# Kernel optimization log

Measured on AMD Instinct MI355X. Metric: run time of the kernel, lower is better.

The kernel has to match this reference:

```python
import jax, jax.numpy as jnp
import numpy as np

BN_EPS = 1e-5

def _haar_details(x):
    # pywt.dwt2(x, 'haar') details for even H, W.
    # Block [[p, q], [r, s]] with p = x[2i,2j], q = x[2i,2j+1], r = x[2i+1,2j], s = x[2i+1,2j+1].
    # cH ('da'): detail along rows, approx along cols; cV ('ad'); cD ('dd').
    B, C, H, W = x.shape
    xb = x.reshape(B, C, H // 2, 2, W // 2, 2)
    p = xb[:, :, :, 0, :, 0]
    q = xb[:, :, :, 0, :, 1]
    r = xb[:, :, :, 1, :, 0]
    s = xb[:, :, :, 1, :, 1]
    cH = (p + q - r - s) * 0.5
    cV = (p - q + r - s) * 0.5
    cD = (p - q - r + s) * 0.5
    return cH, cV, cD

def setup_inputs() -> dict:
    key = jax.random.key(0)
    k1, k2 = jax.random.split(key)
    B, C, H, W = 8, 256, 128, 128
    x = jax.random.normal(k1, (B, C, H, W), dtype=jnp.float32)
    conv_w = jax.random.normal(k2, (C, 4 * C), dtype=jnp.float32) * (1.0 / np.sqrt(4 * C))
    gamma = jnp.ones((C,), dtype=jnp.float32)
    beta = jnp.zeros((C,), dtype=jnp.float32)
    return {"x": x, "conv_w": conv_w, "gamma": gamma, "beta": beta}

def reference(x, conv_w, gamma, beta):
    B, C, H, W = x.shape
    # Original detaches the wavelet branch (CPU numpy path) -> stop_gradient.
    xs = jax.lax.stop_gradient(x)
    cH, cV, cD = _haar_details(xs)
    # Bilinear upsample to (H, W); jax.image.resize bilinear == torch align_corners=False.
    up = lambda t: jax.image.resize(t, (B, C, H, W), method="bilinear")
    enhanced = jnp.concatenate([x, up(cH), up(cV), up(cD)], axis=1)  # [B, 4C, H, W]
    # 1x1 conv, no bias.
    y = jnp.einsum("bchw,oc->bohw", enhanced, conv_w)  # [B, C, H, W]
    # BatchNorm2d, training-mode (batch statistics, biased variance).
    mean = jnp.mean(y, axis=(0, 2, 3), keepdims=True)
    var = jnp.mean((y - mean) ** 2, axis=(0, 2, 3), keepdims=True)
    y_hat = (y - mean) * jax.lax.rsqrt(var + BN_EPS)
    out = jax.nn.relu(y_hat * gamma[None, :, None, None] + beta[None, :, None, None])
    return out
```

## Files before the change

### kernel.cpp

```cpp
#include <hip/hip_runtime.h>
#include <hip/hip_bf16.h>

typedef __bf16 bf16;
typedef __bf16 bf16x8 __attribute__((ext_vector_type(8)));
typedef float  f32x4  __attribute__((ext_vector_type(4)));

#define AS1 __attribute__((address_space(1)))
#define AS3 __attribute__((address_space(3)))

__device__ __forceinline__ void load16_to_lds(const bf16* g, bf16* l) {
    __builtin_amdgcn_global_load_lds((const AS1 unsigned int*)g,
                                     (AS3 unsigned int*)l, 16, 0, 0);
}

__global__ __launch_bounds__(256) void prep_w(const float* __restrict__ w,
                                              bf16* __restrict__ wb) {
    int i = blockIdx.x * 256 + threadIdx.x;
    wb[i] = (bf16)w[i];
}

__global__ __launch_bounds__(256) void pass0(const float* __restrict__ x,
                                             bf16* __restrict__ xt,
                                             bf16* __restrict__ cT) {
    __shared__ bf16 tile[64 * 264];
    const int bid = blockIdx.x;
    const int wt = bid & 3, j = (bid >> 2) & 63, b = bid >> 8;
    const int t = threadIdx.x;
    const int w0 = wt * 32;

    for (int i = 0; i < 16; ++i) {
        int g = i * 256 + t;
        int c = g >> 4;
        int rem = g & 15;
        int dlt = rem >> 3, w4 = rem & 7;
        const float4 v = *(const float4*)(x +
            ((((size_t)b * 256 + c) * 128 + (2 * j + dlt)) * 128 + w0 + w4 * 4));
        int pos = dlt * 32 + w4 * 4;
        tile[(pos + 0) * 264 + c] = (bf16)v.x;
        tile[(pos + 1) * 264 + c] = (bf16)v.y;
        tile[(pos + 2) * 264 + c] = (bf16)v.z;
        tile[(pos + 3) * 264 + c] = (bf16)v.w;
    }
    __syncthreads();

    for (int i = 0; i < 8; ++i) {
        int q = i * 256 + t;
        int cq = q & 31, pos = q >> 5;
        int dlt = pos >> 5, w = pos & 31;
        bf16x8 v = *(const bf16x8*)&tile[pos * 264 + cq * 8];
        int h = 2 * j + dlt, wg = w0 + w;
        *(bf16x8*)(xt + (((size_t)b * 16384 + h * 128 + wg) * 256 + cq * 8)) = v;
    }

    for (int i = 0; i < 2; ++i) {
        int q = i * 256 + t;
        int cq = q & 31, kc = q >> 5;
        bf16x8 vp = *(const bf16x8*)&tile[(2 * kc) * 264 + cq * 8];
        bf16x8 vq = *(const bf16x8*)&tile[(2 * kc + 1) * 264 + cq * 8];
        bf16x8 vr = *(const bf16x8*)&tile[(32 + 2 * kc) * 264 + cq * 8];
        bf16x8 vs = *(const bf16x8*)&tile[(33 + 2 * kc) * 264 + cq * 8];
        bf16x8 oh, ov, od;
        #pragma unroll
        for (int e = 0; e < 8; ++e) {
            float p = (float)vp[e], qq = (float)vq[e];
            float r = (float)vr[e], s = (float)vs[e];
            oh[e] = (bf16)(0.5f * (p + qq - r - s));
            ov[e] = (bf16)(0.5f * (p - qq + r - s));
            od[e] = (bf16)(0.5f * (p - qq - r + s));
        }
        size_t row = ((size_t)b * 4096 + j * 64 + wt * 16 + kc) * 768;
        *(bf16x8*)(cT + row + 0 * 256 + cq * 8) = oh;
        *(bf16x8*)(cT + row + 1 * 256 + cq * 8) = ov;
        *(bf16x8*)(cT + row + 2 * 256 + cq * 8) = od;
    }
}

__global__ __launch_bounds__(256) void gemm_bt(const bf16* __restrict__ W,
                                               const bf16* __restrict__ X,
                                               bf16* __restrict__ Y,
                                               int K, int kofs, int mshift) {
    __shared__ bf16 Wt[128 * 32];
    __shared__ bf16 Xt[128 * 32];
    const int t = threadIdx.x;
    const int wave = t >> 6, lane = t & 63;
    const int quad = lane >> 4, l16 = lane & 15;
    const int m0 = blockIdx.x * 128, o0 = blockIdx.y * 128;
    const int wo = (wave >> 1) * 64, wm = (wave & 1) * 64;
    const int Mplane = 1 << mshift;
    const int r_in = lane >> 2;
    const int cch = lane & 3;

    f32x4 acc[4][4] = {};

    const bf16* wbase = W + (size_t)o0 * 1024 + kofs;
    const bf16* xbase = X + (size_t)m0 * K;

    for (int kk = 0; kk < K; kk += 32) {
        #pragma unroll
        for (int i = 0; i < 2; ++i) {
            int rblk = wave * 2 + i;
            int row = rblk * 16 + r_in;
            load16_to_lds(wbase + (size_t)row * 1024 + kk + cch * 8,
                          &Wt[rblk * 512 + lane * 8]);
            load16_to_lds(xbase + (size_t)row * K + kk + cch * 8,
                          &Xt[rblk * 512 + lane * 8]);
        }
        __syncthreads();
        bf16x8 af[4], bfr[4];
        #pragma unroll
        for (int i = 0; i < 4; ++i)
            af[i] = *(const bf16x8*)&Wt[(wo + i * 16 + l16) * 32 + quad * 8];
        #pragma unroll
        for (int jj = 0; jj < 4; ++jj)
            bfr[jj] = *(const bf16x8*)&Xt[(wm + jj * 16 + l16) * 32 + quad * 8];
        #pragma unroll
        for (int i = 0; i < 4; ++i)
            #pragma unroll
            for (int jj = 0; jj < 4; ++jj)
                acc[i][jj] = __builtin_amdgcn_mfma_f32_16x16x32_bf16(
                    af[i], bfr[jj], acc[i][jj], 0, 0, 0);
        __syncthreads();
    }

    #pragma unroll
    for (int i = 0; i < 4; ++i) {
        int o = o0 + wo + i * 16 + quad * 4;
        #pragma unroll
        for (int jj = 0; jj < 4; ++jj) {
            int m = m0 + wm + jj * 16 + l16;
            int bb = m >> mshift;
            int mp = m & (Mplane - 1);
            bf16* yp = Y + ((size_t)bb * 256 + o) * Mplane + mp;
            #pragma unroll
            for (int r = 0; r < 4; ++r)
                yp[(size_t)r * Mplane] = (bf16)acc[i][jj][r];
        }
    }
}

__device__ __forceinline__ float up_val(const float* zs, int p) {
    int h = p >> 7, w = p & 127;
    int j0 = h >> 1, k0 = w >> 1;
    int jn = (h & 1) ? min(j0 + 1, 63) : max(j0 - 1, 0);
    int kn = (w & 1) ? min(k0 + 1, 63) : max(k0 - 1, 0);
    float zmm = zs[j0 * 64 + k0], zmn = zs[j0 * 64 + kn];
    float znm = zs[jn * 64 + k0], znn = zs[jn * 64 + kn];
    return 0.5625f * zmm + 0.1875f * (zmn + znm) + 0.0625f * znn;
}

__device__ __forceinline__ void load_zplane(const bf16* zp, float* zs, int t) {
    for (int i = 0; i < 2; ++i) {
        int idx = (i * 256 + t) * 8;
        bf16x8 v = *(const bf16x8*)(zp + idx);
        #pragma unroll
        for (int e = 0; e < 8; ++e) zs[idx + e] = (float)v[e];
    }
}

__global__ __launch_bounds__(256) void stats_k(const bf16* __restrict__ y1,
                                               const bf16* __restrict__ z,
                                               float* __restrict__ stats) {
    __shared__ float zs[4096];
    __shared__ float red[8];
    const int bid = blockIdx.x;
    const int o = bid & 255, b = bid >> 8;
    const int t = threadIdx.x;
    const bf16* zp = z + ((size_t)b * 256 + o) * 4096;
    const bf16* yp = y1 + ((size_t)b * 256 + o) * 16384;
    load_zplane(zp, zs, t);
    __syncthreads();
    float s = 0.f, ss = 0.f;
    for (int i = 0; i < 64; ++i) {
        int p = i * 256 + t;
        float y = (float)yp[p] + up_val(zs, p);
        s += y; ss += y * y;
    }
    #pragma unroll
    for (int off = 32; off > 0; off >>= 1) {
        s += __shfl_down(s, off);
        ss += __shfl_down(ss, off);
    }
    if ((t & 63) == 0) { red[t >> 6] = s; red[4 + (t >> 6)] = ss; }
    __syncthreads();
    if (t == 0) {
        atomicAdd(&stats[o],       red[0] + red[1] + red[2] + red[3]);
        atomicAdd(&stats[256 + o], red[4] + red[5] + red[6] + red[7]);
    }
}

__global__ __launch_bounds__(256) void finalize_k(float* __restrict__ stats,
                                                  const float* __restrict__ gamma,
                                                  const float* __restrict__ beta) {
    int o = threadIdx.x;
    const float n = 131072.f;
    float mean = stats[o] / n;
    float var = stats[256 + o] / n - mean * mean;
    float rstd = rsqrtf(var + 1e-5f);
    float sc = rstd * gamma[o];
    stats[512 + o] = sc;
    stats[768 + o] = beta[o] - mean * sc;
}

__global__ __launch_bounds__(256) void apply_k(const bf16* __restrict__ y1,
                                               const bf16* __restrict__ z,
                                               const float* __restrict__ stats,
                                               float* __restrict__ out) {
    __shared__ float zs[4096];
    const int bid = blockIdx.x;
    const int o = bid & 255, b = bid >> 8;
    const int t = threadIdx.x;
    const bf16* zp = z + ((size_t)b * 256 + o) * 4096;
    const bf16* yp = y1 + ((size_t)b * 256 + o) * 16384;
    float* op = out + ((size_t)b * 256 + o) * 16384;
    const float sc = stats[512 + o], sh = stats[768 + o];
    load_zplane(zp, zs, t);
    __syncthreads();
    for (int i = 0; i < 64; ++i) {
        int p = i * 256 + t;
        float y = (float)yp[p] + up_val(zs, p);
        op[p] = fmaxf(fmaf(y, sc, sh), 0.f);
    }
}

extern "C" void kernel_launch(void* const* d_in, const int* in_sizes, int n_in,
                              void* d_out, int out_size, void* d_ws, size_t ws_size,
                              hipStream_t stream) {
    const float* x      = (const float*)d_in[0];
    const float* conv_w = (const float*)d_in[1];
    const float* gamma  = (const float*)d_in[2];
    const float* beta   = (const float*)d_in[3];
    float* out = (float*)d_out;

    char* ws = (char*)d_ws;
    bf16*  Wbf   = (bf16*)ws;
    bf16*  xt    = (bf16*)(ws + (512ll << 10));
    bf16*  z     = (bf16*)(ws + (512ll << 10) + (64ll << 20));
    float* stats = (float*)(ws + (512ll << 10) + (80ll << 20));
    bf16*  shared_reg = (bf16*)(ws + (512ll << 10) + (80ll << 20) + 4096);
    bf16*  cT = shared_reg;
    bf16*  y1 = shared_reg;

    hipMemsetAsync(stats, 0, 4096, stream);
    prep_w<<<1024, 256, 0, stream>>>(conv_w, Wbf);
    pass0<<<2048, 256, 0, stream>>>(x, xt, cT);
    gemm_bt<<<dim3(256, 2), 256, 0, stream>>>(Wbf, cT, z, 768, 256, 12);
    gemm_bt<<<dim3(1024, 2), 256, 0, stream>>>(Wbf, xt, y1, 256, 0, 14);
    stats_k<<<2048, 256, 0, stream>>>(y1, z, stats);
    finalize_k<<<1, 256, 0, stream>>>(stats, gamma, beta);
    apply_k<<<2048, 256, 0, stream>>>(y1, z, stats, out);
}
```

Measured before the change: 353.2 us.

## Merge weight prep and GEMM launches, vectorize epilogue and upsample loops

```diff
diff --git a/kernel.cpp b/kernel.cpp
--- a/kernel.cpp
+++ b/kernel.cpp
@@ -2,6 +2,7 @@
 #include <hip/hip_bf16.h>
 
 typedef __bf16 bf16;
+typedef __bf16 bf16x4 __attribute__((ext_vector_type(4)));
 typedef __bf16 bf16x8 __attribute__((ext_vector_type(8)));
 typedef float  f32x4  __attribute__((ext_vector_type(4)));
 
@@ -13,19 +14,22 @@
                                      (AS3 unsigned int*)l, 16, 0, 0);
 }
 
-__global__ __launch_bounds__(256) void prep_w(const float* __restrict__ w,
-                                              bf16* __restrict__ wb) {
-    int i = blockIdx.x * 256 + threadIdx.x;
-    wb[i] = (bf16)w[i];
-}
-
 __global__ __launch_bounds__(256) void pass0(const float* __restrict__ x,
+                                             const float* __restrict__ cw,
+                                             bf16* __restrict__ wb,
                                              bf16* __restrict__ xt,
                                              bf16* __restrict__ cT) {
     __shared__ bf16 tile[64 * 264];
     const int bid = blockIdx.x;
+    const int t = threadIdx.x;
+    if (bid >= 2048) {
+        int idx = ((bid - 2048) * 256 + t) * 4;
+        const float4 v = *(const float4*)(cw + idx);
+        bf16x4 o; o[0]=(bf16)v.x; o[1]=(bf16)v.y; o[2]=(bf16)v.z; o[3]=(bf16)v.w;
+        *(bf16x4*)(wb + idx) = o;
+        return;
+    }
     const int wt = bid & 3, j = (bid >> 2) & 63, b = bid >> 8;
-    const int t = threadIdx.x;
     const int w0 = wt * 32;
 
     for (int i = 0; i < 16; ++i) {
@@ -75,16 +79,26 @@
     }
 }
 
-__global__ __launch_bounds__(256) void gemm_bt(const bf16* __restrict__ W,
-                                               const bf16* __restrict__ X,
-                                               bf16* __restrict__ Y,
-                                               int K, int kofs, int mshift) {
+__global__ __launch_bounds__(256) void gemm_all(const bf16* __restrict__ W,
+                                                const bf16* __restrict__ cT,
+                                                const bf16* __restrict__ xt,
+                                                bf16* __restrict__ z,
+                                                bf16* __restrict__ y1) {
     __shared__ bf16 Wt[128 * 32];
     __shared__ bf16 Xt[128 * 32];
+    const int bid = blockIdx.x;
+    const bf16* X; bf16* Y; int K, kofs, mshift, m0, o0;
+    if (bid < 512) {
+        K = 768; kofs = 256; mshift = 12; X = cT; Y = z;
+        m0 = (bid & 255) * 128; o0 = (bid >> 8) * 128;
+    } else {
+        int b1 = bid - 512;
+        K = 256; kofs = 0; mshift = 14; X = xt; Y = y1;
+        m0 = (b1 & 1023) * 128; o0 = (b1 >> 10) * 128;
+    }
     const int t = threadIdx.x;
     const int wave = t >> 6, lane = t & 63;
     const int quad = lane >> 4, l16 = lane & 15;
-    const int m0 = blockIdx.x * 128, o0 = blockIdx.y * 128;
     const int wo = (wave >> 1) * 64, wm = (wave & 1) * 64;
     const int Mplane = 1 << mshift;
     const int r_in = lane >> 2;
@@ -118,49 +132,60 @@
             #pragma unroll
             for (int jj = 0; jj < 4; ++jj)
                 acc[i][jj] = __builtin_amdgcn_mfma_f32_16x16x32_bf16(
-                    af[i], bfr[jj], acc[i][jj], 0, 0, 0);
+                    bfr[jj], af[i], acc[i][jj], 0, 0, 0);
         __syncthreads();
     }
 
     #pragma unroll
     for (int i = 0; i < 4; ++i) {
-        int o = o0 + wo + i * 16 + quad * 4;
+        int o = o0 + wo + i * 16 + l16;
         #pragma unroll
         for (int jj = 0; jj < 4; ++jj) {
-            int m = m0 + wm + jj * 16 + l16;
+            int m = m0 + wm + jj * 16 + quad * 4;
             int bb = m >> mshift;
             int mp = m & (Mplane - 1);
-            bf16* yp = Y + ((size_t)bb * 256 + o) * Mplane + mp;
+            bf16x4 v;
             #pragma unroll
-            for (int r = 0; r < 4; ++r)
-                yp[(size_t)r * Mplane] = (bf16)acc[i][jj][r];
-        }
-    }
-}
-
-__device__ __forceinline__ float up_val(const float* zs, int p) {
-    int h = p >> 7, w = p & 127;
-    int j0 = h >> 1, k0 = w >> 1;
-    int jn = (h & 1) ? min(j0 + 1, 63) : max(j0 - 1, 0);
-    int kn = (w & 1) ? min(k0 + 1, 63) : max(k0 - 1, 0);
-    float zmm = zs[j0 * 64 + k0], zmn = zs[j0 * 64 + kn];
-    float znm = zs[jn * 64 + k0], znn = zs[jn * 64 + kn];
-    return 0.5625f * zmm + 0.1875f * (zmn + znm) + 0.0625f * znn;
+            for (int r = 0; r < 4; ++r) v[r] = (bf16)acc[i][jj][r];
+            *(bf16x4*)(Y + ((size_t)bb * 256 + o) * Mplane + mp) = v;
+        }
+    }
 }
 
 __device__ __forceinline__ void load_zplane(const bf16* zp, float* zs, int t) {
     for (int i = 0; i < 2; ++i) {
         int idx = (i * 256 + t) * 8;
+        int j = idx >> 6, k = idx & 63;
         bf16x8 v = *(const bf16x8*)(zp + idx);
         #pragma unroll
-        for (int e = 0; e < 8; ++e) zs[idx + e] = (float)v[e];
+        for (int e = 0; e < 8; ++e) zs[j * 65 + k + e] = (float)v[e];
+    }
+}
+
+__device__ __forceinline__ void up8(const float* zs, int base, float* u) {
+    int h = base >> 7, w0 = base & 127;
+    int j0 = h >> 1;
+    int jn = (h & 1) ? min(j0 + 1, 63) : max(j0 - 1, 0);
+    int K = w0 >> 1;
+    float z0[6], z1[6];
+    #pragma unroll
+    for (int d = 0; d < 6; ++d) {
+        int kc = min(max(K - 1 + d, 0), 63);
+        z0[d] = zs[j0 * 65 + kc];
+        z1[d] = zs[jn * 65 + kc];
+    }
+    #pragma unroll
+    for (int e = 0; e < 8; ++e) {
+        int a = (e >> 1) + 1;
+        int bb = (e & 1) ? a + 1 : a - 1;
+        u[e] = 0.5625f * z0[a] + 0.1875f * (z0[bb] + z1[a]) + 0.0625f * z1[bb];
     }
 }
 
 __global__ __launch_bounds__(256) void stats_k(const bf16* __restrict__ y1,
                                                const bf16* __restrict__ z,
                                                float* __restrict__ stats) {
-    __shared__ float zs[4096];
+    __shared__ float zs[64 * 65];
     __shared__ float red[8];
     const int bid = blockIdx.x;
     const int o = bid & 255, b = bid >> 8;
@@ -170,10 +195,16 @@
     load_zplane(zp, zs, t);
     __syncthreads();
     float s = 0.f, ss = 0.f;
-    for (int i = 0; i < 64; ++i) {
-        int p = i * 256 + t;
-        float y = (float)yp[p] + up_val(zs, p);
-        s += y; ss += y * y;
+    for (int i = 0; i < 8; ++i) {
+        int base = (i * 256 + t) * 8;
+        float u[8];
+        up8(zs, base, u);
+        bf16x8 yv = *(const bf16x8*)(yp + base);
+        #pragma unroll
+        for (int e = 0; e < 8; ++e) {
+            float y = (float)yv[e] + u[e];
+            s += y; ss += y * y;
+        }
     }
     #pragma unroll
     for (int off = 32; off > 0; off >>= 1) {
@@ -205,7 +236,7 @@
                                                const bf16* __restrict__ z,
                                                const float* __restrict__ stats,
                                                float* __restrict__ out) {
-    __shared__ float zs[4096];
+    __shared__ float zs[64 * 65];
     const int bid = blockIdx.x;
     const int o = bid & 255, b = bid >> 8;
     const int t = threadIdx.x;
@@ -215,10 +246,22 @@
     const float sc = stats[512 + o], sh = stats[768 + o];
     load_zplane(zp, zs, t);
     __syncthreads();
-    for (int i = 0; i < 64; ++i) {
-        int p = i * 256 + t;
-        float y = (float)yp[p] + up_val(zs, p);
-        op[p] = fmaxf(fmaf(y, sc, sh), 0.f);
+    for (int i = 0; i < 8; ++i) {
+        int base = (i * 256 + t) * 8;
+        float u[8];
+        up8(zs, base, u);
+        bf16x8 yv = *(const bf16x8*)(yp + base);
+        float4 o0, o1;
+        o0.x = fmaxf(fmaf((float)yv[0] + u[0], sc, sh), 0.f);
+        o0.y = fmaxf(fmaf((float)yv[1] + u[1], sc, sh), 0.f);
+        o0.z = fmaxf(fmaf((float)yv[2] + u[2], sc, sh), 0.f);
+        o0.w = fmaxf(fmaf((float)yv[3] + u[3], sc, sh), 0.f);
+        o1.x = fmaxf(fmaf((float)yv[4] + u[4], sc, sh), 0.f);
+        o1.y = fmaxf(fmaf((float)yv[5] + u[5], sc, sh), 0.f);
+        o1.z = fmaxf(fmaf((float)yv[6] + u[6], sc, sh), 0.f);
+        o1.w = fmaxf(fmaf((float)yv[7] + u[7], sc, sh), 0.f);
+        *(float4*)(op + base) = o0;
+        *(float4*)(op + base + 4) = o1;
     }
 }
 
@@ -236,15 +279,12 @@
     bf16*  xt    = (bf16*)(ws + (512ll << 10));
     bf16*  z     = (bf16*)(ws + (512ll << 10) + (64ll << 20));
     float* stats = (float*)(ws + (512ll << 10) + (80ll << 20));
-    bf16*  shared_reg = (bf16*)(ws + (512ll << 10) + (80ll << 20) + 4096);
-    bf16*  cT = shared_reg;
-    bf16*  y1 = shared_reg;
+    bf16*  cT    = (bf16*)(ws + (512ll << 10) + (80ll << 20) + 4096);
+    bf16*  y1    = (bf16*)(ws + (512ll << 10) + (128ll << 20) + 4096);
 
     hipMemsetAsync(stats, 0, 4096, stream);
-    prep_w<<<1024, 256, 0, stream>>>(conv_w, Wbf);
-    pass0<<<2048, 256, 0, stream>>>(x, xt, cT);
-    gemm_bt<<<dim3(256, 2), 256, 0, stream>>>(Wbf, cT, z, 768, 256, 12);
-    gemm_bt<<<dim3(1024, 2), 256, 0, stream>>>(Wbf, xt, y1, 256, 0, 14);
+    pass0<<<2304, 256, 0, stream>>>(x, conv_w, Wbf, xt, cT);
+    gemm_all<<<2560, 256, 0, stream>>>(Wbf, cT, xt, z, y1);
     stats_k<<<2048, 256, 0, stream>>>(y1, z, stats);
     finalize_k<<<1, 256, 0, stream>>>(stats, gamma, beta);
     apply_k<<<2048, 256, 0, stream>>>(y1, z, stats, out);
```

Result: no change. 352.0 us (-0.3%).
